# Kernel tuning notes

Measured on AMD Instinct MI355X. Metric: run time of the kernel, lower is better.

The kernel has to match this reference:

```python
import jax, jax.numpy as jnp
import numpy as np

B, N, C_IN, C_OUT, K = 8, 1024, 64, 64, 4


def setup_inputs() -> dict:
    key = jax.random.key(0)
    k1, k2, k3 = jax.random.split(key, 3)
    x = jax.random.normal(k1, (B, N, C_IN), dtype=jnp.float32)
    # scaled-Laplacian-like matrix; 1/sqrt(N) scaling keeps Chebyshev recurrence stable
    L = jax.random.normal(k2, (B, N, N), dtype=jnp.float32) * (1.0 / np.sqrt(N))
    theta = jax.random.normal(k3, (K, C_IN, C_OUT), dtype=jnp.float32) * np.sqrt(2.0 / C_IN)
    return {"x": x, "L": L, "theta": theta}


def reference(x, L, theta):
    # Chebyshev recurrence applied directly to feature vectors:
    #   z0 = x, z1 = L x, z_k = 2 L z_{k-1} - z_{k-2}
    # out = sum_k z_k @ theta[k]  -- same math as materializing T_k(L),
    # since T_k(L) @ x obeys the same 3-term recurrence.
    k_orders = theta.shape[0]
    z_prev = x                      # [B,N,C]
    out = jnp.matmul(z_prev, theta[0])
    if k_orders > 1:
        z_curr = jnp.matmul(L, x)   # [B,N,C]
        out = out + jnp.matmul(z_curr, theta[1])
        for k in range(2, k_orders):
            z_next = 2.0 * jnp.matmul(L, z_curr) - z_prev
            out = out + jnp.matmul(z_next, theta[k])
            z_prev, z_curr = z_curr, z_next
    return out
```

## Files before the change

kernel.cpp:

```cpp
#include <hip/hip_runtime.h>
#include <cstdint>
#include <cstddef>


typedef __bf16 bf16;
typedef bf16 bf16x8 __attribute__((ext_vector_type(8)));
typedef bf16 bf16x4 __attribute__((ext_vector_type(4)));
typedef float f32x4 __attribute__((ext_vector_type(4)));

#define MFMA_BF16(a, b, c) __builtin_amdgcn_mfma_f32_16x16x32_bf16((a), (b), (c), 0, 0, 0)

__global__ __launch_bounds__(256) void prep_kernel(const float* __restrict__ x,
                                                   const float* __restrict__ theta,
                                                   bf16* __restrict__ xT,
                                                   bf16* __restrict__ thT)
{
    __shared__ bf16 tile[64][72];
    const int bid = blockIdx.x;
    const float* src;
    bf16* dst;
    int dst_ld;
    if (bid < 128) {
        const int b = bid >> 4;
        const int n0 = (bid & 15) << 6;
        src = x + ((size_t)(b * 1024 + n0)) * 64;
        dst = xT + (size_t)b * 64 * 1024 + n0;
        dst_ld = 1024;
    } else {
        const int k = bid - 128;
        src = theta + (size_t)k * 4096;
        dst = thT + (size_t)k * 4096;
        dst_ld = 64;
    }
    const int t = threadIdx.x;
    const int r = t >> 2;
    const int c0 = (t & 3) << 4;
#pragma unroll
    for (int j = 0; j < 16; j += 4) {
        f32x4 v = *reinterpret_cast<const f32x4*>(src + r * 64 + c0 + j);
        tile[r][c0 + j + 0] = (bf16)v[0];
        tile[r][c0 + j + 1] = (bf16)v[1];
        tile[r][c0 + j + 2] = (bf16)v[2];
        tile[r][c0 + j + 3] = (bf16)v[3];
    }
    __syncthreads();
    bf16x8 o0, o1;
#pragma unroll
    for (int j = 0; j < 8; ++j) {
        o0[j] = tile[c0 + j][r];
        o1[j] = tile[c0 + 8 + j][r];
    }
    *reinterpret_cast<bf16x8*>(dst + (size_t)r * dst_ld + c0) = o0;
    *reinterpret_cast<bf16x8*>(dst + (size_t)r * dst_ld + c0 + 8) = o1;
}

template <int STAGE>
__global__ __launch_bounds__(256) void stage_kernel(
    const float* __restrict__ Lmat,
    const float* __restrict__ x,
    const bf16* __restrict__ zinT,
    const bf16* __restrict__ zprevT,
    const bf16* __restrict__ thT,
    bf16* __restrict__ zoutT,
    float* __restrict__ out)
{
    __shared__ bf16 A_lds[32 * 72];

    const int bid = blockIdx.x;
    const int b  = bid >> 5;
    const int m0 = (bid & 31) << 5;
    const int t  = threadIdx.x;
    const int w  = t >> 6;
    const int l  = t & 63;
    const int l15 = l & 15;
    const int lg  = l >> 4;

    const float* Lb  = Lmat + (size_t)b * (1024 * 1024);
    const bf16*  zin = zinT + (size_t)b * (64 * 1024);

    const int sr = t >> 3;
    const int sc = (t & 7) << 3;
    const float* lrow = Lb + (size_t)(m0 + sr) * 1024 + sc;
    const bf16* bptr = zin + (size_t)(w * 16 + l15) * 1024 + lg * 8;

    f32x4 acc0 = {0.f, 0.f, 0.f, 0.f};
    f32x4 acc1 = {0.f, 0.f, 0.f, 0.f};

    f32x4 av0 = *reinterpret_cast<const f32x4*>(lrow + 0);
    f32x4 av1 = *reinterpret_cast<const f32x4*>(lrow + 4);

    for (int k0 = 0; k0 < 1024; k0 += 64) {
        bf16x8 bfr0 = *reinterpret_cast<const bf16x8*>(bptr + k0);
        bf16x8 bfr1 = *reinterpret_cast<const bf16x8*>(bptr + k0 + 32);
        f32x4 nv0, nv1;
        if (k0 + 64 < 1024) {
            nv0 = *reinterpret_cast<const f32x4*>(lrow + k0 + 64);
            nv1 = *reinterpret_cast<const f32x4*>(lrow + k0 + 68);
        }
        __syncthreads();
        bf16x8 apk;
        apk[0] = (bf16)av0[0]; apk[1] = (bf16)av0[1];
        apk[2] = (bf16)av0[2]; apk[3] = (bf16)av0[3];
        apk[4] = (bf16)av1[0]; apk[5] = (bf16)av1[1];
        apk[6] = (bf16)av1[2]; apk[7] = (bf16)av1[3];
        *reinterpret_cast<bf16x8*>(&A_lds[sr * 72 + sc]) = apk;
        __syncthreads();
        bf16x8 a00 = *reinterpret_cast<const bf16x8*>(&A_lds[(l15) * 72 + lg * 8]);
        bf16x8 a01 = *reinterpret_cast<const bf16x8*>(&A_lds[(l15) * 72 + 32 + lg * 8]);
        bf16x8 a10 = *reinterpret_cast<const bf16x8*>(&A_lds[(16 + l15) * 72 + lg * 8]);
        bf16x8 a11 = *reinterpret_cast<const bf16x8*>(&A_lds[(16 + l15) * 72 + 32 + lg * 8]);
        acc0 = MFMA_BF16(a00, bfr0, acc0);
        acc0 = MFMA_BF16(a01, bfr1, acc0);
        acc1 = MFMA_BF16(a10, bfr0, acc1);
        acc1 = MFMA_BF16(a11, bfr1, acc1);
        av0 = nv0;
        av1 = nv1;
    }

    const int c = w * 16 + l15;
    const float alpha = (STAGE == 1) ? 1.0f : 2.0f;
    f32x4 z0v, z1v;
    {
        f32x4 zp0 = {0.f, 0.f, 0.f, 0.f};
        f32x4 zp1 = {0.f, 0.f, 0.f, 0.f};
        if constexpr (STAGE >= 2) {
            const bf16* zpb = zprevT + (size_t)(b * 64 + c) * 1024 + m0 + lg * 4;
            bf16x4 p0 = *reinterpret_cast<const bf16x4*>(zpb);
            bf16x4 p1 = *reinterpret_cast<const bf16x4*>(zpb + 16);
#pragma unroll
            for (int r = 0; r < 4; ++r) { zp0[r] = (float)p0[r]; zp1[r] = (float)p1[r]; }
        }
#pragma unroll
        for (int r = 0; r < 4; ++r) {
            z0v[r] = alpha * acc0[r] - zp0[r];
            z1v[r] = alpha * acc1[r] - zp1[r];
        }
    }
    if constexpr (STAGE <= 2) {
        bf16* zob = zoutT + (size_t)(b * 64 + c) * 1024 + m0 + lg * 4;
        bf16x4 q0, q1;
#pragma unroll
        for (int r = 0; r < 4; ++r) { q0[r] = (bf16)z0v[r]; q1[r] = (bf16)z1v[r]; }
        *reinterpret_cast<bf16x4*>(zob) = q0;
        *reinterpret_cast<bf16x4*>(zob + 16) = q1;
    }

    __syncthreads();
#pragma unroll
    for (int r = 0; r < 4; ++r) {
        A_lds[(lg * 4 + r) * 72 + c]      = (bf16)z0v[r];
        A_lds[(16 + lg * 4 + r) * 72 + c] = (bf16)z1v[r];
    }
    __syncthreads();

    f32x4 oa0, oa1;
    if constexpr (STAGE == 1) {
        oa0 = (f32x4){0.f, 0.f, 0.f, 0.f};
        oa1 = (f32x4){0.f, 0.f, 0.f, 0.f};
#pragma unroll
        for (int ck = 0; ck < 2; ++ck) {
            bf16x8 bt = *reinterpret_cast<const bf16x8*>(
                thT + (size_t)(0 * 64 + w * 16 + l15) * 64 + ck * 32 + lg * 8);
            const float* xp0 = x + (size_t)(b * 1024 + m0 + l15) * 64 + ck * 32 + lg * 8;
            const float* xp1 = xp0 + (size_t)16 * 64;
            f32x4 u0 = *reinterpret_cast<const f32x4*>(xp0);
            f32x4 u1 = *reinterpret_cast<const f32x4*>(xp0 + 4);
            f32x4 v0 = *reinterpret_cast<const f32x4*>(xp1);
            f32x4 v1 = *reinterpret_cast<const f32x4*>(xp1 + 4);
            bf16x8 ax0, ax1;
#pragma unroll
            for (int j = 0; j < 4; ++j) {
                ax0[j] = (bf16)u0[j]; ax0[4 + j] = (bf16)u1[j];
                ax1[j] = (bf16)v0[j]; ax1[4 + j] = (bf16)v1[j];
            }
            oa0 = MFMA_BF16(ax0, bt, oa0);
            oa1 = MFMA_BF16(ax1, bt, oa1);
        }
    } else {
#pragma unroll
        for (int r = 0; r < 4; ++r) {
            oa0[r] = out[(size_t)(b * 1024 + m0 + lg * 4 + r) * 64 + w * 16 + l15];
            oa1[r] = out[(size_t)(b * 1024 + m0 + 16 + lg * 4 + r) * 64 + w * 16 + l15];
        }
    }
    constexpr int KTH = (STAGE == 1) ? 1 : STAGE;
#pragma unroll
    for (int ck = 0; ck < 2; ++ck) {
        bf16x8 bt = *reinterpret_cast<const bf16x8*>(
            thT + (size_t)(KTH * 64 + w * 16 + l15) * 64 + ck * 32 + lg * 8);
        bf16x8 az0 = *reinterpret_cast<const bf16x8*>(&A_lds[l15 * 72 + ck * 32 + lg * 8]);
        bf16x8 az1 = *reinterpret_cast<const bf16x8*>(&A_lds[(16 + l15) * 72 + ck * 32 + lg * 8]);
        oa0 = MFMA_BF16(az0, bt, oa0);
        oa1 = MFMA_BF16(az1, bt, oa1);
    }
#pragma unroll
    for (int r = 0; r < 4; ++r) {
        out[(size_t)(b * 1024 + m0 + lg * 4 + r) * 64 + w * 16 + l15]      = oa0[r];
        out[(size_t)(b * 1024 + m0 + 16 + lg * 4 + r) * 64 + w * 16 + l15] = oa1[r];
    }
}

extern "C" void kernel_launch(void* const* d_in, const int* in_sizes, int n_in,
                              void* d_out, int out_size, void* d_ws, size_t ws_size,
                              hipStream_t stream)
{
    const float* x  = (const float*)d_in[0];
    const float* L  = (const float*)d_in[1];
    const float* th = (const float*)d_in[2];
    float* out = (float*)d_out;

    bf16* xT  = (bf16*)d_ws;
    bf16* z1T = xT  + (size_t)8 * 64 * 1024;
    bf16* z2T = z1T + (size_t)8 * 64 * 1024;
    bf16* thT = z2T + (size_t)8 * 64 * 1024;

    prep_kernel<<<dim3(132), dim3(256), 0, stream>>>(x, th, xT, thT);
    stage_kernel<1><<<dim3(256), dim3(256), 0, stream>>>(L, x, xT, xT, thT, z1T, out);
    stage_kernel<2><<<dim3(256), dim3(256), 0, stream>>>(L, x, z1T, xT, thT, z2T, out);
    stage_kernel<3><<<dim3(256), dim3(256), 0, stream>>>(L, x, z2T, z1T, thT, z2T, out);
}
```

Measured before the change: 108.0 us.

## Swap MFMA operand roles, drop LDS staging of L, deep register prefetch

The L·z matmul now feeds L straight from global memory into registers as the MFMA B operand, and z^T acts as the A operand, which removes the LDS staging and the two barriers per k-step. An 8-deep register prefetch pipeline keeps several loads in flight. Tiles shrink to 16 rows, so the grid doubles to 512 blocks. Stage 1 also reads a bf16 copy of x written by the prep kernel instead of converting fp32 x. The cost is higher register pressure, and each wave now reads the full L rows independently, so L is loaded redundantly across the four waves of a block.

```diff
diff --git a/kernel.cpp b/kernel.cpp
--- a/kernel.cpp
+++ b/kernel.cpp
@@ -5,7 +5,6 @@
 
 typedef __bf16 bf16;
 typedef bf16 bf16x8 __attribute__((ext_vector_type(8)));
-typedef bf16 bf16x4 __attribute__((ext_vector_type(4)));
 typedef float f32x4 __attribute__((ext_vector_type(4)));
 
 #define MFMA_BF16(a, b, c) __builtin_amdgcn_mfma_f32_16x16x32_bf16((a), (b), (c), 0, 0, 0)
@@ -13,191 +12,162 @@
 __global__ __launch_bounds__(256) void prep_kernel(const float* __restrict__ x,
                                                    const float* __restrict__ theta,
                                                    bf16* __restrict__ xT,
+                                                   bf16* __restrict__ xb,
                                                    bf16* __restrict__ thT)
 {
     __shared__ bf16 tile[64][72];
     const int bid = blockIdx.x;
+    const int t = threadIdx.x;
+    const int r = t >> 2;
+    const int c0 = (t & 3) << 4;
+
     const float* src;
-    bf16* dst;
+    bf16* dstT;
     int dst_ld;
-    if (bid < 128) {
-        const int b = bid >> 4;
-        const int n0 = (bid & 15) << 6;
-        src = x + ((size_t)(b * 1024 + n0)) * 64;
-        dst = xT + (size_t)b * 64 * 1024 + n0;
+    const bool isx = bid < 128;
+    int b = 0, n0 = 0;
+    if (isx) {
+        b = bid >> 4; n0 = (bid & 15) << 6;
+        src = x + (size_t)(b * 1024 + n0) * 64;
+        dstT = xT + (size_t)b * 64 * 1024 + n0;
         dst_ld = 1024;
     } else {
         const int k = bid - 128;
         src = theta + (size_t)k * 4096;
-        dst = thT + (size_t)k * 4096;
+        dstT = thT + (size_t)k * 4096;
         dst_ld = 64;
     }
-    const int t = threadIdx.x;
-    const int r = t >> 2;
-    const int c0 = (t & 3) << 4;
+
+    bf16x8 row0, row1;
 #pragma unroll
     for (int j = 0; j < 16; j += 4) {
         f32x4 v = *reinterpret_cast<const f32x4*>(src + r * 64 + c0 + j);
-        tile[r][c0 + j + 0] = (bf16)v[0];
-        tile[r][c0 + j + 1] = (bf16)v[1];
-        tile[r][c0 + j + 2] = (bf16)v[2];
-        tile[r][c0 + j + 3] = (bf16)v[3];
+#pragma unroll
+        for (int i = 0; i < 4; ++i) {
+            bf16 q = (bf16)v[i];
+            tile[r][c0 + j + i] = q;
+            if (j + i < 8) row0[j + i] = q; else row1[j + i - 8] = q;
+        }
+    }
+    if (isx) {
+        bf16* xr = xb + (size_t)(b * 1024 + n0 + r) * 64 + c0;
+        *reinterpret_cast<bf16x8*>(xr) = row0;
+        *reinterpret_cast<bf16x8*>(xr + 8) = row1;
     }
     __syncthreads();
     bf16x8 o0, o1;
 #pragma unroll
-    for (int j = 0; j < 8; ++j) {
-        o0[j] = tile[c0 + j][r];
-        o1[j] = tile[c0 + 8 + j][r];
-    }
-    *reinterpret_cast<bf16x8*>(dst + (size_t)r * dst_ld + c0) = o0;
-    *reinterpret_cast<bf16x8*>(dst + (size_t)r * dst_ld + c0 + 8) = o1;
+    for (int j = 0; j < 8; ++j) { o0[j] = tile[c0 + j][r]; o1[j] = tile[c0 + 8 + j][r]; }
+    *reinterpret_cast<bf16x8*>(dstT + (size_t)r * dst_ld + c0) = o0;
+    *reinterpret_cast<bf16x8*>(dstT + (size_t)r * dst_ld + c0 + 8) = o1;
 }
 
 template <int STAGE>
 __global__ __launch_bounds__(256) void stage_kernel(
     const float* __restrict__ Lmat,
-    const float* __restrict__ x,
+    const bf16* __restrict__ xb,
     const bf16* __restrict__ zinT,
     const bf16* __restrict__ zprevT,
     const bf16* __restrict__ thT,
     bf16* __restrict__ zoutT,
     float* __restrict__ out)
 {
-    __shared__ bf16 A_lds[32 * 72];
+    __shared__ __align__(16) bf16 zbuf[16][72];
 
     const int bid = blockIdx.x;
-    const int b  = bid >> 5;
-    const int m0 = (bid & 31) << 5;
+    const int b  = bid >> 6;
+    const int m0 = (bid & 63) << 4;
     const int t  = threadIdx.x;
     const int w  = t >> 6;
     const int l  = t & 63;
     const int l15 = l & 15;
     const int lg  = l >> 4;
+    const int c0  = w << 4;
 
-    const float* Lb  = Lmat + (size_t)b * (1024 * 1024);
-    const bf16*  zin = zinT + (size_t)b * (64 * 1024);
+    const bf16*  aptr = zinT + (size_t)(b * 64 + c0 + l15) * 1024 + lg * 8;
+    const float* bptr = Lmat + (size_t)(b * 1024 + m0 + l15) * 1024 + lg * 8;
 
-    const int sr = t >> 3;
-    const int sc = (t & 7) << 3;
-    const float* lrow = Lb + (size_t)(m0 + sr) * 1024 + sc;
-    const bf16* bptr = zin + (size_t)(w * 16 + l15) * 1024 + lg * 8;
+    f32x4 acc = {0.f, 0.f, 0.f, 0.f};
 
-    f32x4 acc0 = {0.f, 0.f, 0.f, 0.f};
-    f32x4 acc1 = {0.f, 0.f, 0.f, 0.f};
-
-    f32x4 av0 = *reinterpret_cast<const f32x4*>(lrow + 0);
-    f32x4 av1 = *reinterpret_cast<const f32x4*>(lrow + 4);
-
-    for (int k0 = 0; k0 < 1024; k0 += 64) {
-        bf16x8 bfr0 = *reinterpret_cast<const bf16x8*>(bptr + k0);
-        bf16x8 bfr1 = *reinterpret_cast<const bf16x8*>(bptr + k0 + 32);
-        f32x4 nv0, nv1;
-        if (k0 + 64 < 1024) {
-            nv0 = *reinterpret_cast<const f32x4*>(lrow + k0 + 64);
-            nv1 = *reinterpret_cast<const f32x4*>(lrow + k0 + 68);
+    constexpr int DEPTH = 8;
+    bf16x8 aR[DEPTH];
+    f32x4  b0R[DEPTH], b1R[DEPTH];
+#pragma unroll
+    for (int u = 0; u < DEPTH; ++u) {
+        aR[u]  = *reinterpret_cast<const bf16x8*>(aptr + u * 32);
+        b0R[u] = *reinterpret_cast<const f32x4*>(bptr + u * 32);
+        b1R[u] = *reinterpret_cast<const f32x4*>(bptr + u * 32 + 4);
+    }
+    for (int k0 = 0; k0 < 1024 - 32 * DEPTH; k0 += 32 * DEPTH) {
+#pragma unroll
+        for (int u = 0; u < DEPTH; ++u) {
+            bf16x8 bb;
+#pragma unroll
+            for (int j = 0; j < 4; ++j) { bb[j] = (bf16)b0R[u][j]; bb[4 + j] = (bf16)b1R[u][j]; }
+            bf16x8 av = aR[u];
+            const int kn = k0 + 32 * DEPTH + u * 32;
+            aR[u]  = *reinterpret_cast<const bf16x8*>(aptr + kn);
+            b0R[u] = *reinterpret_cast<const f32x4*>(bptr + kn);
+            b1R[u] = *reinterpret_cast<const f32x4*>(bptr + kn + 4);
+            acc = MFMA_BF16(av, bb, acc);
         }
-        __syncthreads();
-        bf16x8 apk;
-        apk[0] = (bf16)av0[0]; apk[1] = (bf16)av0[1];
-        apk[2] = (bf16)av0[2]; apk[3] = (bf16)av0[3];
-        apk[4] = (bf16)av1[0]; apk[5] = (bf16)av1[1];
-        apk[6] = (bf16)av1[2]; apk[7] = (bf16)av1[3];
-        *reinterpret_cast<bf16x8*>(&A_lds[sr * 72 + sc]) = apk;
-        __syncthreads();
-        bf16x8 a00 = *reinterpret_cast<const bf16x8*>(&A_lds[(l15) * 72 + lg * 8]);
-        bf16x8 a01 = *reinterpret_cast<const bf16x8*>(&A_lds[(l15) * 72 + 32 + lg * 8]);
-        bf16x8 a10 = *reinterpret_cast<const bf16x8*>(&A_lds[(16 + l15) * 72 + lg * 8]);
-        bf16x8 a11 = *reinterpret_cast<const bf16x8*>(&A_lds[(16 + l15) * 72 + 32 + lg * 8]);
-        acc0 = MFMA_BF16(a00, bfr0, acc0);
-        acc0 = MFMA_BF16(a01, bfr1, acc0);
-        acc1 = MFMA_BF16(a10, bfr0, acc1);
-        acc1 = MFMA_BF16(a11, bfr1, acc1);
-        av0 = nv0;
-        av1 = nv1;
+    }
+#pragma unroll
+    for (int u = 0; u < DEPTH; ++u) {
+        bf16x8 bb;
+#pragma unroll
+        for (int j = 0; j < 4; ++j) { bb[j] = (bf16)b0R[u][j]; bb[4 + j] = (bf16)b1R[u][j]; }
+        acc = MFMA_BF16(aR[u], bb, acc);
     }
 
-    const int c = w * 16 + l15;
+    const int cr = c0 + lg * 4;
     const float alpha = (STAGE == 1) ? 1.0f : 2.0f;
-    f32x4 z0v, z1v;
-    {
-        f32x4 zp0 = {0.f, 0.f, 0.f, 0.f};
-        f32x4 zp1 = {0.f, 0.f, 0.f, 0.f};
-        if constexpr (STAGE >= 2) {
-            const bf16* zpb = zprevT + (size_t)(b * 64 + c) * 1024 + m0 + lg * 4;
-            bf16x4 p0 = *reinterpret_cast<const bf16x4*>(zpb);
-            bf16x4 p1 = *reinterpret_cast<const bf16x4*>(zpb + 16);
+    float zv[4];
 #pragma unroll
-            for (int r = 0; r < 4; ++r) { zp0[r] = (float)p0[r]; zp1[r] = (float)p1[r]; }
-        }
-#pragma unroll
-        for (int r = 0; r < 4; ++r) {
-            z0v[r] = alpha * acc0[r] - zp0[r];
-            z1v[r] = alpha * acc1[r] - zp1[r];
-        }
+    for (int r = 0; r < 4; ++r) {
+        float zp = 0.f;
+        if constexpr (STAGE >= 2)
+            zp = (float)zprevT[(size_t)(b * 64 + cr + r) * 1024 + m0 + l15];
+        zv[r] = alpha * acc[r] - zp;
     }
     if constexpr (STAGE <= 2) {
-        bf16* zob = zoutT + (size_t)(b * 64 + c) * 1024 + m0 + lg * 4;
-        bf16x4 q0, q1;
 #pragma unroll
-        for (int r = 0; r < 4; ++r) { q0[r] = (bf16)z0v[r]; q1[r] = (bf16)z1v[r]; }
-        *reinterpret_cast<bf16x4*>(zob) = q0;
-        *reinterpret_cast<bf16x4*>(zob + 16) = q1;
+        for (int r = 0; r < 4; ++r)
+            zoutT[(size_t)(b * 64 + cr + r) * 1024 + m0 + l15] = (bf16)zv[r];
     }
-
-    __syncthreads();
 #pragma unroll
-    for (int r = 0; r < 4; ++r) {
-        A_lds[(lg * 4 + r) * 72 + c]      = (bf16)z0v[r];
-        A_lds[(16 + lg * 4 + r) * 72 + c] = (bf16)z1v[r];
-    }
+    for (int r = 0; r < 4; ++r)
+        zbuf[l15][cr + r] = (bf16)zv[r];
     __syncthreads();
 
-    f32x4 oa0, oa1;
+    const int o = (w << 4) + l15;
+    f32x4 oacc;
     if constexpr (STAGE == 1) {
-        oa0 = (f32x4){0.f, 0.f, 0.f, 0.f};
-        oa1 = (f32x4){0.f, 0.f, 0.f, 0.f};
+        oacc = (f32x4){0.f, 0.f, 0.f, 0.f};
 #pragma unroll
         for (int ck = 0; ck < 2; ++ck) {
+            bf16x8 ax = *reinterpret_cast<const bf16x8*>(
+                xb + (size_t)(b * 1024 + m0 + l15) * 64 + ck * 32 + lg * 8);
             bf16x8 bt = *reinterpret_cast<const bf16x8*>(
-                thT + (size_t)(0 * 64 + w * 16 + l15) * 64 + ck * 32 + lg * 8);
-            const float* xp0 = x + (size_t)(b * 1024 + m0 + l15) * 64 + ck * 32 + lg * 8;
-            const float* xp1 = xp0 + (size_t)16 * 64;
-            f32x4 u0 = *reinterpret_cast<const f32x4*>(xp0);
-            f32x4 u1 = *reinterpret_cast<const f32x4*>(xp0 + 4);
-            f32x4 v0 = *reinterpret_cast<const f32x4*>(xp1);
-            f32x4 v1 = *reinterpret_cast<const f32x4*>(xp1 + 4);
-            bf16x8 ax0, ax1;
-#pragma unroll
-            for (int j = 0; j < 4; ++j) {
-                ax0[j] = (bf16)u0[j]; ax0[4 + j] = (bf16)u1[j];
-                ax1[j] = (bf16)v0[j]; ax1[4 + j] = (bf16)v1[j];
-            }
-            oa0 = MFMA_BF16(ax0, bt, oa0);
-            oa1 = MFMA_BF16(ax1, bt, oa1);
+                thT + (size_t)o * 64 + ck * 32 + lg * 8);
+            oacc = MFMA_BF16(ax, bt, oacc);
         }
     } else {
 #pragma unroll
-        for (int r = 0; r < 4; ++r) {
-            oa0[r] = out[(size_t)(b * 1024 + m0 + lg * 4 + r) * 64 + w * 16 + l15];
-            oa1[r] = out[(size_t)(b * 1024 + m0 + 16 + lg * 4 + r) * 64 + w * 16 + l15];
-        }
+        for (int r = 0; r < 4; ++r)
+            oacc[r] = out[(size_t)(b * 1024 + m0 + lg * 4 + r) * 64 + o];
     }
     constexpr int KTH = (STAGE == 1) ? 1 : STAGE;
 #pragma unroll
     for (int ck = 0; ck < 2; ++ck) {
+        bf16x8 az = *reinterpret_cast<const bf16x8*>(&zbuf[l15][ck * 32 + lg * 8]);
         bf16x8 bt = *reinterpret_cast<const bf16x8*>(
-            thT + (size_t)(KTH * 64 + w * 16 + l15) * 64 + ck * 32 + lg * 8);
-        bf16x8 az0 = *reinterpret_cast<const bf16x8*>(&A_lds[l15 * 72 + ck * 32 + lg * 8]);
-        bf16x8 az1 = *reinterpret_cast<const bf16x8*>(&A_lds[(16 + l15) * 72 + ck * 32 + lg * 8]);
-        oa0 = MFMA_BF16(az0, bt, oa0);
-        oa1 = MFMA_BF16(az1, bt, oa1);
+            thT + (size_t)(KTH * 64 + o) * 64 + ck * 32 + lg * 8);
+        oacc = MFMA_BF16(az, bt, oacc);
     }
 #pragma unroll
-    for (int r = 0; r < 4; ++r) {
-        out[(size_t)(b * 1024 + m0 + lg * 4 + r) * 64 + w * 16 + l15]      = oa0[r];
-        out[(size_t)(b * 1024 + m0 + 16 + lg * 4 + r) * 64 + w * 16 + l15] = oa1[r];
-    }
+    for (int r = 0; r < 4; ++r)
+        out[(size_t)(b * 1024 + m0 + lg * 4 + r) * 64 + o] = oacc[r];
 }
 
 extern "C" void kernel_launch(void* const* d_in, const int* in_sizes, int n_in,
@@ -210,12 +180,14 @@
     float* out = (float*)d_out;
 
     bf16* xT  = (bf16*)d_ws;
-    bf16* z1T = xT  + (size_t)8 * 64 * 1024;
+    bf16* xb  = xT  + (size_t)8 * 64 * 1024;
+    bf16* z1T = xb  + (size_t)8 * 64 * 1024;
+    bf16* z1b = nullptr; (void)z1b;
     bf16* z2T = z1T + (size_t)8 * 64 * 1024;
     bf16* thT = z2T + (size_t)8 * 64 * 1024;
 
-    prep_kernel<<<dim3(132), dim3(256), 0, stream>>>(x, th, xT, thT);
-    stage_kernel<1><<<dim3(256), dim3(256), 0, stream>>>(L, x, xT, xT, thT, z1T, out);
-    stage_kernel<2><<<dim3(256), dim3(256), 0, stream>>>(L, x, z1T, xT, thT, z2T, out);
-    stage_kernel<3><<<dim3(256), dim3(256), 0, stream>>>(L, x, z2T, z1T, thT, z2T, out);
+    prep_kernel<<<dim3(132), dim3(256), 0, stream>>>(x, th, xT, xb, thT);
+    stage_kernel<1><<<dim3(512), dim3(256), 0, stream>>>(L, xb, xT, xT, thT, z1T, out);
+    stage_kernel<2><<<dim3(512), dim3(256), 0, stream>>>(L, xb, z1T, xT, thT, z2T, out);
+    stage_kernel<3><<<dim3(512), dim3(256), 0, stream>>>(L, xb, z2T, z1T, thT, nullptr, out);
 }
```

New measurement: 149.6 us. 38.5% more time.
